# Kernel tuning notes

Measured on AMD Instinct MI355X. Metric: run time of the kernel, lower is better.

## Reference

```python
import jax, jax.numpy as jnp
import numpy as np

SEQ, BATCH, IN, HID, OUT = 512, 64, 512, 1024, 512
KEEP = 0.7  # dropout p = 0.3


def setup_inputs() -> dict:
    key = jax.random.key(0)
    ks = jax.random.split(key, 9)
    def lin(k, fan_out, fan_in):
        bound = 1.0 / np.sqrt(fan_in)
        kw, kb = jax.random.split(k)
        W = jax.random.uniform(kw, (fan_out, fan_in), jnp.float32, -bound, bound)
        b = jax.random.uniform(kb, (fan_out,), jnp.float32, -bound, bound)
        return W, b
    x = jax.random.normal(ks[0], (SEQ, BATCH, IN), jnp.float32)
    # inverted dropout mask, fixed for determinism
    drop_mask = (jax.random.bernoulli(ks[1], KEEP, (SEQ, BATCH, OUT))
                 .astype(jnp.float32) / KEEP)
    W_i2h, b_i2h = lin(ks[2], HID, IN + HID)
    W_i2o, b_i2o = lin(ks[3], OUT, IN + HID)
    W_o2o, b_o2o = lin(ks[4], OUT, HID + OUT)
    return {"x": x, "drop_mask": drop_mask,
            "W_i2h": W_i2h, "b_i2h": b_i2h,
            "W_i2o": W_i2o, "b_i2o": b_i2o,
            "W_o2o": W_o2o, "b_o2o": b_o2o}


def reference(x, drop_mask, W_i2h, b_i2h, W_i2o, b_i2o, W_o2o, b_o2o):
    # x: [S, B, IN]; returns log-probs [S, B, OUT]
    def step(h, inp):
        x_t, m_t = inp  # [B, IN], [B, OUT]
        comb = jnp.concatenate([x_t, h], axis=1)          # [B, IN+HID]
        out = comb @ W_i2o.T + b_i2o                      # [B, OUT]
        h_new = comb @ W_i2h.T + b_i2h                    # [B, HID]
        oc = jnp.concatenate([out, h_new], axis=1) @ W_o2o.T + b_o2o  # [B, OUT]
        oc = oc * m_t                                     # dropout (inverted mask)
        oc = jax.nn.log_softmax(oc, axis=-1)
        return h_new, oc
    h0 = jnp.zeros((x.shape[1], W_i2h.shape[0]), x.dtype)
    _, outs = jax.lax.scan(step, h0, (x, drop_mask))
    return outs
```

## Files before the change

### kernel.cpp

```cpp
#include <hip/hip_runtime.h>
#include <stdint.h>


typedef unsigned short ushort_t;
typedef __attribute__((ext_vector_type(8))) __bf16 bf16x8;
typedef __attribute__((ext_vector_type(4))) float f32x4;

__device__ __forceinline__ ushort_t f2bf(float f) {
  union { float f; uint32_t u; } v; v.f = f;
  uint32_t r = v.u + 0x7fffu + ((v.u >> 16) & 1u);
  return (ushort_t)(r >> 16);
}
__device__ __forceinline__ float bf2f(ushort_t b) {
  union { uint32_t u; float f; } v; v.u = ((uint32_t)b) << 16;
  return v.f;
}
__device__ __forceinline__ void gload16(const ushort_t* g, ushort_t* l) {
  __builtin_amdgcn_global_load_lds(
      (const __attribute__((address_space(1))) uint32_t*)g,
      (__attribute__((address_space(3))) uint32_t*)l, 16, 0, 0);
}

__global__ __launch_bounds__(256) void init_kernel(uint32_t* harr0) {
  int i = blockIdx.x * blockDim.x + threadIdx.x;
  if (i < 32768) harr0[i] = 0;
}

__global__ __launch_bounds__(256) void pack_kernel(
    const float* __restrict__ x, const float* __restrict__ mask,
    const float* __restrict__ W_i2h,
    const float* __restrict__ W_i2o, const float* __restrict__ W_o2o,
    const float* __restrict__ b_i2o, const float* __restrict__ b_o2o,
    ushort_t* xB, ushort_t* Wihx, ushort_t* Whh, ushort_t* Wiox,
    ushort_t* Wioh, ushort_t* Wo1, ushort_t* Wo2, float* biasP,
    uint64_t* maskb) {
  int64_t i = (int64_t)blockIdx.x * blockDim.x + threadIdx.x;
  const int64_t c0 = 16777216, c1 = 17301504, c2 = 18350080, c3 = 18612224,
                c4 = 19136512, c5 = 19398656, c6 = 19922944, c7 = 19923456,
                c8 = 36700672;
  if (i < c0) { xB[i] = f2bf(x[i]); return; }
  if (i < c1) { int64_t j = i - c0; int r = j >> 9,  c = j & 511;  Wihx[j] = f2bf(W_i2h[(int64_t)r * 1536 + c]); return; }
  if (i < c2) { int64_t j = i - c1; int r = j >> 10, c = j & 1023; Whh[j]  = f2bf(W_i2h[(int64_t)r * 1536 + 512 + c]); return; }
  if (i < c3) { int64_t j = i - c2; int r = j >> 9,  c = j & 511;  Wiox[j] = f2bf(W_i2o[(int64_t)r * 1536 + c]); return; }
  if (i < c4) { int64_t j = i - c3; int r = j >> 10, c = j & 1023; Wioh[j] = f2bf(W_i2o[(int64_t)r * 1536 + 512 + c]); return; }
  if (i < c5) { int64_t j = i - c4; int r = j >> 9,  c = j & 511;  Wo1[j]  = f2bf(W_o2o[(int64_t)r * 1536 + c]); return; }
  if (i < c6) { int64_t j = i - c5; int r = j >> 10, c = j & 1023; Wo2[j]  = f2bf(W_o2o[(int64_t)r * 1536 + 512 + c]); return; }
  if (i < c7) {
    int n = (int)(i - c6);
    const float* wr = W_o2o + (int64_t)n * 1536;
    float s = 0.f;
    for (int m = 0; m < 512; ++m) s += wr[m] * b_i2o[m];
    biasP[n] = s + b_o2o[n];
    return;
  }
  if (i < c8) {
    int64_t j = i - c7;
    float v = mask[j];
    uint64_t bits = __ballot(v != 0.0f);
    if ((j & 63) == 0) maskb[j >> 6] = bits;
  }
}

__global__ __launch_bounds__(256) void gemm_bt(
    const ushort_t* __restrict__ A1, int lda1, const ushort_t* __restrict__ B1, int K1,
    const float* __restrict__ bias, ushort_t* Cb, int Ntiles) {
  __shared__ __align__(16) ushort_t AsF[2][4096];
  __shared__ __align__(16) ushort_t BsF[2][4096];
  const int mt = blockIdx.x & 255, nt = blockIdx.x >> 8;
  const int m0 = mt * 128, n0 = nt * 128;
  const int tid = threadIdx.x;
  const int w = tid >> 6, l = tid & 63;
  const int quad = l >> 4, l15 = l & 15;
  const int wm = (w & 1) * 64, wn = (w >> 1) * 64;
  const int r0 = tid >> 2, chunk = tid & 3;
  f32x4 acc[4][4] = {};
  gload16(A1 + (size_t)(m0 + r0) * lda1 + chunk * 8,      &AsF[0][tid * 8]);
  gload16(A1 + (size_t)(m0 + r0 + 64) * lda1 + chunk * 8, &AsF[0][2048 + tid * 8]);
  gload16(B1 + (size_t)(n0 + r0) * K1 + chunk * 8,        &BsF[0][tid * 8]);
  gload16(B1 + (size_t)(n0 + r0 + 64) * K1 + chunk * 8,   &BsF[0][2048 + tid * 8]);
  const int NIT = K1 >> 5;
  for (int it = 0; it < NIT; ++it) {
    const int p = it & 1;
    __syncthreads();
    if (it + 1 < NIT) {
      const int kn = (it + 1) * 32;
      gload16(A1 + (size_t)(m0 + r0) * lda1 + kn + chunk * 8,      &AsF[p ^ 1][tid * 8]);
      gload16(A1 + (size_t)(m0 + r0 + 64) * lda1 + kn + chunk * 8, &AsF[p ^ 1][2048 + tid * 8]);
      gload16(B1 + (size_t)(n0 + r0) * K1 + kn + chunk * 8,        &BsF[p ^ 1][tid * 8]);
      gload16(B1 + (size_t)(n0 + r0 + 64) * K1 + kn + chunk * 8,   &BsF[p ^ 1][2048 + tid * 8]);
    }
    bf16x8 af[4], bfr[4];
#pragma unroll
    for (int i = 0; i < 4; ++i) af[i]  = *(const bf16x8*)&AsF[p][(wm + 16 * i + l15) * 32 + 8 * quad];
#pragma unroll
    for (int j = 0; j < 4; ++j) bfr[j] = *(const bf16x8*)&BsF[p][(wn + 16 * j + l15) * 32 + 8 * quad];
#pragma unroll
    for (int i = 0; i < 4; ++i)
#pragma unroll
      for (int j = 0; j < 4; ++j)
        acc[i][j] = __builtin_amdgcn_mfma_f32_16x16x32_bf16(af[i], bfr[j], acc[i][j], 0, 0, 0);
  }
  const int N = Ntiles * 128;
#pragma unroll
  for (int i = 0; i < 4; ++i) {
    const int row = m0 + wm + 16 * i + 4 * quad;
#pragma unroll
    for (int j = 0; j < 4; ++j) {
      const int col = n0 + wn + 16 * j + l15;
      const float bv = bias[col];
#pragma unroll
      for (int r = 0; r < 4; ++r)
        Cb[(size_t)(row + r) * N + col] = f2bf(acc[i][j][r] + bv);
    }
  }
}

__global__ __launch_bounds__(256) void usetup_kernel(
    const ushort_t* __restrict__ Wo1, const ushort_t* __restrict__ Wiox,
    const ushort_t* __restrict__ Wioh, ushort_t* __restrict__ U1,
    ushort_t* __restrict__ U2) {
  __shared__ __align__(16) ushort_t AsF[4096];
  __shared__ __align__(16) ushort_t BsF[4096];
  int job = blockIdx.x;
  const ushort_t* Bm; ushort_t* Om; int mt, nt, ldb;
  if (job < 16) { mt = job >> 2; nt = job & 3; Bm = Wiox; Om = U1; ldb = 512; }
  else { job -= 16; mt = job >> 3; nt = job & 7; Bm = Wioh; Om = U2; ldb = 1024; }
  const int m0 = mt * 128, n0 = nt * 128;
  const int tid = threadIdx.x;
  const int w = tid >> 6, l = tid & 63;
  const int quad = l >> 4, l15 = l & 15;
  const int wm = (w & 1) * 64, wn = (w >> 1) * 64;
  const int r0 = tid >> 2, chunk = tid & 3;
  f32x4 acc[4][4] = {};
  for (int k0 = 0; k0 < 512; k0 += 32) {
    __syncthreads();
    gload16(Wo1 + (size_t)(m0 + r0) * 512 + k0 + chunk * 8,      &AsF[tid * 8]);
    gload16(Wo1 + (size_t)(m0 + r0 + 64) * 512 + k0 + chunk * 8, &AsF[2048 + tid * 8]);
#pragma unroll
    for (int rep = 0; rep < 2; ++rep) {
      const int idx = tid + 256 * rep;
      const int kk = idx & 31, n8 = idx >> 5;
      union { uint4 v; ushort_t s[8]; } u;
      u.v = *(const uint4*)(Bm + (size_t)(k0 + kk) * ldb + n0 + n8 * 8);
#pragma unroll
      for (int i = 0; i < 8; ++i) BsF[(n8 * 8 + i) * 32 + kk] = u.s[i];
    }
    __syncthreads();
    bf16x8 af[4], bfr[4];
#pragma unroll
    for (int i = 0; i < 4; ++i) af[i]  = *(const bf16x8*)&AsF[(wm + 16 * i + l15) * 32 + 8 * quad];
#pragma unroll
    for (int j = 0; j < 4; ++j) bfr[j] = *(const bf16x8*)&BsF[(wn + 16 * j + l15) * 32 + 8 * quad];
#pragma unroll
    for (int i = 0; i < 4; ++i)
#pragma unroll
      for (int j = 0; j < 4; ++j)
        acc[i][j] = __builtin_amdgcn_mfma_f32_16x16x32_bf16(af[i], bfr[j], acc[i][j], 0, 0, 0);
  }
#pragma unroll
  for (int i = 0; i < 4; ++i) {
    const int row = m0 + wm + 16 * i + 4 * quad;
#pragma unroll
    for (int j = 0; j < 4; ++j) {
      const int col = n0 + wn + 16 * j + l15;
#pragma unroll
      for (int r = 0; r < 4; ++r)
        Om[(size_t)(row + r) * ldb + col] = f2bf(acc[i][j][r]);
    }
  }
}

__device__ void step_tile64(
    const ushort_t* __restrict__ A, const ushort_t* __restrict__ B, int n0,
    const ushort_t* __restrict__ X, ushort_t* __restrict__ O, int gate) {
  __shared__ __align__(16) ushort_t As[2][2048];
  __shared__ __align__(16) ushort_t Bs[2][4096];
  const int tid = threadIdx.x;
  const int w = tid >> 6, l = tid & 63;
  const int quad = l >> 4, l15 = l & 15;
  const int r0 = tid >> 2, chunk = tid & 3;
  f32x4 acc[4][2] = {};
  gload16(A + (size_t)r0 * 1024 + chunk * 8,             &As[0][tid * 8]);
  gload16(B + (size_t)(n0 + r0) * 1024 + chunk * 8,      &Bs[0][tid * 8]);
  gload16(B + (size_t)(n0 + r0 + 64) * 1024 + chunk * 8, &Bs[0][2048 + tid * 8]);
  for (int k0 = 0; k0 < 32; ++k0) {
    const int p = k0 & 1;
    __syncthreads();
    if (k0 < 31) {
      const int kn = (k0 + 1) * 32;
      gload16(A + (size_t)r0 * 1024 + kn + chunk * 8,             &As[p ^ 1][tid * 8]);
      gload16(B + (size_t)(n0 + r0) * 1024 + kn + chunk * 8,      &Bs[p ^ 1][tid * 8]);
      gload16(B + (size_t)(n0 + r0 + 64) * 1024 + kn + chunk * 8, &Bs[p ^ 1][2048 + tid * 8]);
    }
    bf16x8 af[4], bfr[2];
#pragma unroll
    for (int i = 0; i < 4; ++i) af[i]  = *(const bf16x8*)&As[p][(16 * i + l15) * 32 + 8 * quad];
#pragma unroll
    for (int j = 0; j < 2; ++j) bfr[j] = *(const bf16x8*)&Bs[p][(32 * w + 16 * j + l15) * 32 + 8 * quad];
#pragma unroll
    for (int i = 0; i < 4; ++i)
#pragma unroll
      for (int j = 0; j < 2; ++j)
        acc[i][j] = __builtin_amdgcn_mfma_f32_16x16x32_bf16(af[i], bfr[j], acc[i][j], 0, 0, 0);
  }
#pragma unroll
  for (int i = 0; i < 4; ++i) {
#pragma unroll
    for (int j = 0; j < 2; ++j) {
      const int col = n0 + 32 * w + 16 * j + l15;
#pragma unroll
      for (int r = 0; r < 4; ++r) {
        const int row = 16 * i + 4 * quad + r;
        const size_t idx = (size_t)row * 1024 + col;
        float v = gate ? acc[i][j][r] : 0.0f;
        O[idx] = f2bf(v + bf2f(X[idx]));
      }
    }
  }
}

__device__ void power_tile(const ushort_t* __restrict__ Am,
                           const ushort_t* __restrict__ Bm,
                           ushort_t* __restrict__ Om, int t) {
  __shared__ __align__(16) ushort_t AsF[4096];
  __shared__ __align__(16) ushort_t BsF[4096];
  const int mt = t >> 3, nt = t & 7;
  const int m0 = mt * 128, n0 = nt * 128;
  const int tid = threadIdx.x;
  const int w = tid >> 6, l = tid & 63;
  const int quad = l >> 4, l15 = l & 15;
  const int wm = (w & 1) * 64, wn = (w >> 1) * 64;
  const int r0 = tid >> 2, chunk = tid & 3;
  f32x4 acc[4][4] = {};
  for (int k0 = 0; k0 < 1024; k0 += 32) {
    __syncthreads();
    gload16(Am + (size_t)(m0 + r0) * 1024 + k0 + chunk * 8,      &AsF[tid * 8]);
    gload16(Am + (size_t)(m0 + r0 + 64) * 1024 + k0 + chunk * 8, &AsF[2048 + tid * 8]);
#pragma unroll
    for (int rep = 0; rep < 2; ++rep) {
      const int idx = tid + 256 * rep;
      const int kk = idx & 31, n8 = idx >> 5;
      union { uint4 v; ushort_t s[8]; } u;
      u.v = *(const uint4*)(Bm + (size_t)(k0 + kk) * 1024 + n0 + n8 * 8);
#pragma unroll
      for (int i = 0; i < 8; ++i) BsF[(n8 * 8 + i) * 32 + kk] = u.s[i];
    }
    __syncthreads();
    bf16x8 af[4], bfr[4];
#pragma unroll
    for (int i = 0; i < 4; ++i) af[i]  = *(const bf16x8*)&AsF[(wm + 16 * i + l15) * 32 + 8 * quad];
#pragma unroll
    for (int j = 0; j < 4; ++j) bfr[j] = *(const bf16x8*)&BsF[(wn + 16 * j + l15) * 32 + 8 * quad];
#pragma unroll
    for (int i = 0; i < 4; ++i)
#pragma unroll
      for (int j = 0; j < 4; ++j)
        acc[i][j] = __builtin_amdgcn_mfma_f32_16x16x32_bf16(af[i], bfr[j], acc[i][j], 0, 0, 0);
  }
#pragma unroll
  for (int i = 0; i < 4; ++i) {
    const int row = m0 + wm + 16 * i + 4 * quad;
#pragma unroll
    for (int j = 0; j < 4; ++j) {
      const int col = n0 + wn + 16 * j + l15;
#pragma unroll
      for (int r = 0; r < 4; ++r)
        Om[(size_t)(row + r) * 1024 + col] = f2bf(acc[i][j][r]);
    }
  }
}

#define PWp(idx) (Pw + (size_t)(idx) * 1048576)

__global__ __launch_bounds__(256) void step_pow(
    const ushort_t* __restrict__ A, const ushort_t* __restrict__ X,
    ushort_t* __restrict__ O, const ushort_t* __restrict__ Whh,
    ushort_t* __restrict__ Pw, int mode) {
  const int bid = blockIdx.x;
  if (mode == 8 || bid >= 512) {
    const int q = (mode == 8) ? bid : bid - 512;
    const int pj = q >> 6, t = q & 63;
    const ushort_t *Am, *Bm; ushort_t* Om;
    switch (mode) {
      case 1:  Am = Whh;     Bm = Whh;     Om = PWp(0);  break;
      case 2:  if (pj == 0) { Am = Whh;    Bm = PWp(0);  Om = PWp(1); }
               else         { Am = PWp(0); Bm = PWp(0);  Om = PWp(2); }
               break;
      case 3:  if (pj == 0)      { Am = Whh;    Bm = PWp(2); Om = PWp(3); }
               else if (pj == 1) { Am = PWp(0); Bm = PWp(2); Om = PWp(4); }
               else if (pj == 2) { Am = PWp(1); Bm = PWp(2); Om = PWp(5); }
               else              { Am = PWp(2); Bm = PWp(2); Om = PWp(6); }
               break;
      case 4:  Am = PWp(6);  Bm = PWp(6);  Om = PWp(7);  break;
      case 5:  Am = PWp(7);  Bm = PWp(7);  Om = PWp(8);  break;
      case 6:  Am = PWp(8);  Bm = PWp(8);  Om = PWp(9);  break;
      case 7:  Am = PWp(9);  Bm = PWp(9);  Om = PWp(10); break;
      default: Am = PWp(10); Bm = PWp(10); Om = PWp(11); break;
    }
    power_tile(Am, Bm, Om, t);
    return;
  }
  const int c = bid >> 3, nt = bid & 7;
  step_tile64(A + (size_t)c * 524288, Whh, nt * 128,
              X + (size_t)c * 524288, O + (size_t)c * 524288, 1);
}

__global__ __launch_bounds__(256) void scan64(
    const ushort_t* __restrict__ old, ushort_t* __restrict__ nw,
    const ushort_t* __restrict__ Pv, int d) {
  const int c = blockIdx.x >> 3, nt = blockIdx.x & 7;
  const int ia = (c >= d) ? (c - d) : c;
  step_tile64(old + (size_t)ia * 524288, Pv, nt * 128,
              old + (size_t)c * 524288, nw + (size_t)c * 524288, c >= d);
}

__global__ __launch_bounds__(256) void correct_kernel(
    const ushort_t* __restrict__ S, const ushort_t* __restrict__ XhB,
    ushort_t* __restrict__ Harr, const ushort_t* __restrict__ Whh,
    const ushort_t* __restrict__ Pw) {
  __shared__ __align__(16) ushort_t AsF[2][4096];
  __shared__ __align__(16) ushort_t BsF[2][4096];
  const int p_ = blockIdx.x >> 3;
  const int n0 = (blockIdx.x & 7) * 128;
  const int j = blockIdx.y + 1;
  const ushort_t* Wj = (j == 1) ? Whh : (Pw + (size_t)(j - 2) * 1048576);
  const ushort_t* Xs = (j == 1) ? XhB : (Harr + (size_t)j * 65536);
  ushort_t* XO = Harr + (size_t)j * 65536;
  const int tid = threadIdx.x;
  const int w = tid >> 6, l = tid & 63;
  const int quad = l >> 4, l15 = l & 15;
  const int wm = (w & 1) * 64, wn = (w >> 1) * 64;
  const int r0 = tid >> 2, chunk = tid & 3;
  f32x4 acc[4][4] = {};
  const ushort_t* a0 = S + (size_t)(2 * p_) * 524288 + (size_t)r0 * 1024;
  const ushort_t* a1 = S + (size_t)(2 * p_ + 1) * 524288 + (size_t)r0 * 1024;
  gload16(a0 + chunk * 8, &AsF[0][tid * 8]);
  gload16(a1 + chunk * 8, &AsF[0][2048 + tid * 8]);
  gload16(Wj + (size_t)(n0 + r0) * 1024 + chunk * 8,      &BsF[0][tid * 8]);
  gload16(Wj + (size_t)(n0 + r0 + 64) * 1024 + chunk * 8, &BsF[0][2048 + tid * 8]);
  for (int it = 0; it < 32; ++it) {
    const int p = it & 1;
    __syncthreads();
    if (it < 31) {
      const int kn = (it + 1) * 32;
      gload16(a0 + kn + chunk * 8, &AsF[p ^ 1][tid * 8]);
      gload16(a1 + kn + chunk * 8, &AsF[p ^ 1][2048 + tid * 8]);
      gload16(Wj + (size_t)(n0 + r0) * 1024 + kn + chunk * 8,      &BsF[p ^ 1][tid * 8]);
      gload16(Wj + (size_t)(n0 + r0 + 64) * 1024 + kn + chunk * 8, &BsF[p ^ 1][2048 + tid * 8]);
    }
    bf16x8 af[4], bfr[4];
#pragma unroll
    for (int i = 0; i < 4; ++i) af[i]  = *(const bf16x8*)&AsF[p][(wm + 16 * i + l15) * 32 + 8 * quad];
#pragma unroll
    for (int jj = 0; jj < 4; ++jj) bfr[jj] = *(const bf16x8*)&BsF[p][(wn + 16 * jj + l15) * 32 + 8 * quad];
#pragma unroll
    for (int i = 0; i < 4; ++i)
#pragma unroll
      for (int jj = 0; jj < 4; ++jj)
        acc[i][jj] = __builtin_amdgcn_mfma_f32_16x16x32_bf16(af[i], bfr[jj], acc[i][jj], 0, 0, 0);
  }
#pragma unroll
  for (int i = 0; i < 4; ++i) {
#pragma unroll
    for (int jj = 0; jj < 4; ++jj) {
      const int col = n0 + wn + 16 * jj + l15;
#pragma unroll
      for (int r = 0; r < 4; ++r) {
        const int gr = wm + 16 * i + 4 * quad + r;
        const int c = 2 * p_ + (gr >> 6);
        const size_t idx = (size_t)c * 524288 + (size_t)(gr & 63) * 1024 + col;
        XO[idx] = f2bf(acc[i][jj][r] + bf2f(Xs[idx]));
      }
    }
  }
}

__global__ __launch_bounds__(256) void gemm_fused(
    const ushort_t* __restrict__ xB, const ushort_t* __restrict__ U1,
    const ushort_t* __restrict__ Harr, const ushort_t* __restrict__ U2,
    const ushort_t* __restrict__ Wo2, const float* __restrict__ biasP,
    const uint64_t* __restrict__ maskb, float* __restrict__ out) {
  __shared__ __align__(16) ushort_t AsF[2][4096];
  __shared__ __align__(16) ushort_t BsF[2][4096];
  const int mt = blockIdx.x & 255, nt = blockIdx.x >> 8;
  const int m0 = mt * 128, n0 = nt * 128;
  const int tid = threadIdx.x;
  const int w = tid >> 6, l = tid & 63;
  const int quad = l >> 4, l15 = l & 15;
  const int wm = (w & 1) * 64, wn = (w >> 1) * 64;
  const int r0 = tid >> 2, chunk = tid & 3;
  f32x4 acc[4][4] = {};
  auto issue = [&](int it, int b) {
    const ushort_t *A, *B; int K, k0;
    if (it < 16)      { A = xB;           B = U1;  K = 512;  k0 = it << 5; }
    else if (it < 48) { A = Harr;         B = U2;  K = 1024; k0 = (it - 16) << 5; }
    else              { A = Harr + 65536; B = Wo2; K = 1024; k0 = (it - 48) << 5; }
    gload16(A + (size_t)(m0 + r0) * K + k0 + chunk * 8,      &AsF[b][tid * 8]);
    gload16(A + (size_t)(m0 + r0 + 64) * K + k0 + chunk * 8, &AsF[b][2048 + tid * 8]);
    gload16(B + (size_t)(n0 + r0) * K + k0 + chunk * 8,      &BsF[b][tid * 8]);
    gload16(B + (size_t)(n0 + r0 + 64) * K + k0 + chunk * 8, &BsF[b][2048 + tid * 8]);
  };
  issue(0, 0);
  for (int it = 0; it < 80; ++it) {
    const int p = it & 1;
    __syncthreads();
    if (it < 79) issue(it + 1, p ^ 1);
    bf16x8 af[4], bfr[4];
#pragma unroll
    for (int i = 0; i < 4; ++i) af[i]  = *(const bf16x8*)&AsF[p][(wm + 16 * i + l15) * 32 + 8 * quad];
#pragma unroll
    for (int j = 0; j < 4; ++j) bfr[j] = *(const bf16x8*)&BsF[p][(wn + 16 * j + l15) * 32 + 8 * quad];
#pragma unroll
    for (int i = 0; i < 4; ++i)
#pragma unroll
      for (int j = 0; j < 4; ++j)
        acc[i][j] = __builtin_amdgcn_mfma_f32_16x16x32_bf16(af[i], bfr[j], acc[i][j], 0, 0, 0);
  }
  const float INV_KEEP = 1.0f / 0.7f;
#pragma unroll
  for (int i = 0; i < 4; ++i) {
    const int row = m0 + wm + 16 * i + 4 * quad;
#pragma unroll
    for (int j = 0; j < 4; ++j) {
      const int col = n0 + wn + 16 * j + l15;
      const float bv = biasP[col];
#pragma unroll
      for (int r = 0; r < 4; ++r) {
        const size_t idx = (size_t)(row + r) * 512 + col;
        const uint64_t bits = maskb[idx >> 6];
        out[idx] = ((bits >> (idx & 63)) & 1) ? (acc[i][j][r] + bv) * INV_KEEP
                                              : 0.0f;
      }
    }
  }
}

__global__ __launch_bounds__(256) void softmax_kernel(float* __restrict__ out) {
  const int row = blockIdx.x;
  const int tid = threadIdx.x;
  const size_t base = (size_t)row * 512;
  __shared__ float sm[4], ss[4];
  const float v0 = out[base + tid];
  const float v1 = out[base + tid + 256];
  float m = fmaxf(v0, v1);
#pragma unroll
  for (int off = 32; off; off >>= 1) m = fmaxf(m, __shfl_xor(m, off, 64));
  const int w = tid >> 6;
  if ((tid & 63) == 0) sm[w] = m;
  __syncthreads();
  m = fmaxf(fmaxf(sm[0], sm[1]), fmaxf(sm[2], sm[3]));
  float s = __expf(v0 - m) + __expf(v1 - m);
#pragma unroll
  for (int off = 32; off; off >>= 1) s += __shfl_xor(s, off, 64);
  if ((tid & 63) == 0) ss[w] = s;
  __syncthreads();
  s = ss[0] + ss[1] + ss[2] + ss[3];
  const float lg = logf(s);
  out[base + tid] = v0 - m - lg;
  out[base + tid + 256] = v1 - m - lg;
}

extern "C" void kernel_launch(void* const* d_in, const int* in_sizes, int n_in,
                              void* d_out, int out_size, void* d_ws, size_t ws_size,
                              hipStream_t stream) {
  const float* x     = (const float*)d_in[0];
  const float* mask  = (const float*)d_in[1];
  const float* W_i2h = (const float*)d_in[2];
  const float* b_i2h = (const float*)d_in[3];
  const float* W_i2o = (const float*)d_in[4];
  const float* b_i2o = (const float*)d_in[5];
  const float* W_o2o = (const float*)d_in[6];
  const float* b_o2o = (const float*)d_in[7];
  float* out = (float*)d_out;

  char* ws = (char*)d_ws;
  const size_t NEED = 207749120;
  if (ws_size < NEED) return;
  ushort_t* xB   = (ushort_t*)(ws + 0);
  ushort_t* XhB  = (ushort_t*)(ws + 33554432);
  ushort_t* SA   = XhB + 65536;
  ushort_t* SB   = XhB + 3 * 65536;
  ushort_t* Harr = (ushort_t*)(ws + 100663296);
  ushort_t* Pw   = (ushort_t*)(ws + 167903232);
  ushort_t* U1   = (ushort_t*)(ws + 193069056);
  ushort_t* U2   = (ushort_t*)(ws + 193593344);
  float* biasP   = (float*)(ws + 194641920);
  uint64_t* maskb = (uint64_t*)(ws + 195000320);
  ushort_t* Wihx = (ushort_t*)(ws + 201457664);
  ushort_t* Whh  = (ushort_t*)(ws + 202506240);
  ushort_t* Wiox = (ushort_t*)(ws + 204603392);
  ushort_t* Wioh = (ushort_t*)(ws + 205127680);
  ushort_t* Wo1  = (ushort_t*)(ws + 206176256);
  ushort_t* Wo2  = (ushort_t*)(ws + 206700544);

  hipLaunchKernelGGL(init_kernel, dim3(128), dim3(256), 0, stream, (uint32_t*)Harr);
  hipLaunchKernelGGL(pack_kernel, dim3(143362), dim3(256), 0, stream,
                     x, mask, W_i2h, W_i2o, W_o2o, b_i2o, b_o2o,
                     xB, Wihx, Whh, Wiox, Wioh, Wo1, Wo2, biasP, maskb);
  hipLaunchKernelGGL(gemm_bt, dim3(2048), dim3(256), 0, stream,
                     xB, 512, Wihx, 512, b_i2h, XhB, 8);
  hipLaunchKernelGGL(usetup_kernel, dim3(48), dim3(256), 0, stream,
                     Wo1, Wiox, Wioh, U1, U2);
  const int extraP[8] = {0, 64, 128, 256, 64, 64, 64, 64};
  for (int k = 1; k <= 7; ++k) {
    const ushort_t* A = (k == 1) ? XhB : (Harr + (size_t)k * 65536);
    hipLaunchKernelGGL(step_pow, dim3(512 + extraP[k]), dim3(256), 0, stream,
                       A, XhB + (size_t)k * 65536, Harr + (size_t)(k + 1) * 65536,
                       Whh, Pw, k);
  }
  hipLaunchKernelGGL(step_pow, dim3(64), dim3(256), 0, stream,
                     Whh, Whh, (ushort_t*)Harr, Whh, Pw, 8);
  hipLaunchKernelGGL(scan64, dim3(512), dim3(256), 0, stream, Harr, SB, Pw + 6 * 1048576, 1);
  hipLaunchKernelGGL(scan64, dim3(512), dim3(256), 0, stream, SB, SA, Pw + 7 * 1048576, 2);
  hipLaunchKernelGGL(scan64, dim3(512), dim3(256), 0, stream, SA, SB, Pw + 8 * 1048576, 4);
  hipLaunchKernelGGL(scan64, dim3(512), dim3(256), 0, stream, SB, SA, Pw + 9 * 1048576, 8);
  hipLaunchKernelGGL(scan64, dim3(512), dim3(256), 0, stream, SA, SB, Pw + 10 * 1048576, 16);
  hipLaunchKernelGGL(scan64, dim3(512), dim3(256), 0, stream, SB, SA, Pw + 11 * 1048576, 32);
  hipLaunchKernelGGL(correct_kernel, dim3(dim3(256, 8)), dim3(256), 0, stream,
                     SA, XhB, Harr, Whh, Pw);
  hipLaunchKernelGGL(gemm_fused, dim3(1024), dim3(256), 0, stream,
                     xB, U1, Harr, U2, Wo2, biasP, maskb, out);
  hipLaunchKernelGGL(softmax_kernel, dim3(32768), dim3(256), 0, stream, out);
}
```

Before: 1.035 ms.

## Restructure recurrence into fewer wider passes and fold power GEMMs into scans

Replaces the seven sequential step_pow launches plus a separate power launch with three pass kernels. Each pass computes several hidden-state chunks in parallel using precomputed powers of Whh, with a two-term accumulation where needed. Each later matrix power is folded into the preceding scan launch, the usetup GEMM is merged into gemm_bt, and scan blocks with c<d now do a plain copy instead of a gated zero GEMM. The aim is to shorten the serial kernel chain and cut wasted MFMA work, in exchange for more complex dependency ordering between launches and shared-memory reuse across heterogeneous blocks.

```diff
diff --git a/kernel.cpp b/kernel.cpp
--- a/kernel.cpp
+++ b/kernel.cpp
@@ -61,67 +61,12 @@
   }
 }
 
-__global__ __launch_bounds__(256) void gemm_bt(
-    const ushort_t* __restrict__ A1, int lda1, const ushort_t* __restrict__ B1, int K1,
-    const float* __restrict__ bias, ushort_t* Cb, int Ntiles) {
-  __shared__ __align__(16) ushort_t AsF[2][4096];
-  __shared__ __align__(16) ushort_t BsF[2][4096];
-  const int mt = blockIdx.x & 255, nt = blockIdx.x >> 8;
-  const int m0 = mt * 128, n0 = nt * 128;
-  const int tid = threadIdx.x;
-  const int w = tid >> 6, l = tid & 63;
-  const int quad = l >> 4, l15 = l & 15;
-  const int wm = (w & 1) * 64, wn = (w >> 1) * 64;
-  const int r0 = tid >> 2, chunk = tid & 3;
-  f32x4 acc[4][4] = {};
-  gload16(A1 + (size_t)(m0 + r0) * lda1 + chunk * 8,      &AsF[0][tid * 8]);
-  gload16(A1 + (size_t)(m0 + r0 + 64) * lda1 + chunk * 8, &AsF[0][2048 + tid * 8]);
-  gload16(B1 + (size_t)(n0 + r0) * K1 + chunk * 8,        &BsF[0][tid * 8]);
-  gload16(B1 + (size_t)(n0 + r0 + 64) * K1 + chunk * 8,   &BsF[0][2048 + tid * 8]);
-  const int NIT = K1 >> 5;
-  for (int it = 0; it < NIT; ++it) {
-    const int p = it & 1;
-    __syncthreads();
-    if (it + 1 < NIT) {
-      const int kn = (it + 1) * 32;
-      gload16(A1 + (size_t)(m0 + r0) * lda1 + kn + chunk * 8,      &AsF[p ^ 1][tid * 8]);
-      gload16(A1 + (size_t)(m0 + r0 + 64) * lda1 + kn + chunk * 8, &AsF[p ^ 1][2048 + tid * 8]);
-      gload16(B1 + (size_t)(n0 + r0) * K1 + kn + chunk * 8,        &BsF[p ^ 1][tid * 8]);
-      gload16(B1 + (size_t)(n0 + r0 + 64) * K1 + kn + chunk * 8,   &BsF[p ^ 1][2048 + tid * 8]);
-    }
-    bf16x8 af[4], bfr[4];
-#pragma unroll
-    for (int i = 0; i < 4; ++i) af[i]  = *(const bf16x8*)&AsF[p][(wm + 16 * i + l15) * 32 + 8 * quad];
-#pragma unroll
-    for (int j = 0; j < 4; ++j) bfr[j] = *(const bf16x8*)&BsF[p][(wn + 16 * j + l15) * 32 + 8 * quad];
-#pragma unroll
-    for (int i = 0; i < 4; ++i)
-#pragma unroll
-      for (int j = 0; j < 4; ++j)
-        acc[i][j] = __builtin_amdgcn_mfma_f32_16x16x32_bf16(af[i], bfr[j], acc[i][j], 0, 0, 0);
-  }
-  const int N = Ntiles * 128;
-#pragma unroll
-  for (int i = 0; i < 4; ++i) {
-    const int row = m0 + wm + 16 * i + 4 * quad;
-#pragma unroll
-    for (int j = 0; j < 4; ++j) {
-      const int col = n0 + wn + 16 * j + l15;
-      const float bv = bias[col];
-#pragma unroll
-      for (int r = 0; r < 4; ++r)
-        Cb[(size_t)(row + r) * N + col] = f2bf(acc[i][j][r] + bv);
-    }
-  }
-}
-
-__global__ __launch_bounds__(256) void usetup_kernel(
+__device__ void usetup_tile(ushort_t* SH,
     const ushort_t* __restrict__ Wo1, const ushort_t* __restrict__ Wiox,
     const ushort_t* __restrict__ Wioh, ushort_t* __restrict__ U1,
-    ushort_t* __restrict__ U2) {
-  __shared__ __align__(16) ushort_t AsF[4096];
-  __shared__ __align__(16) ushort_t BsF[4096];
-  int job = blockIdx.x;
+    ushort_t* __restrict__ U2, int job) {
+  ushort_t* AsF = SH;
+  ushort_t* BsF = SH + 4096;
   const ushort_t* Bm; ushort_t* Om; int mt, nt, ldb;
   if (job < 16) { mt = job >> 2; nt = job & 3; Bm = Wiox; Om = U1; ldb = 512; }
   else { job -= 16; mt = job >> 3; nt = job & 7; Bm = Wioh; Om = U2; ldb = 1024; }
@@ -170,33 +115,98 @@
   }
 }
 
-__device__ void step_tile64(
-    const ushort_t* __restrict__ A, const ushort_t* __restrict__ B, int n0,
-    const ushort_t* __restrict__ X, ushort_t* __restrict__ O, int gate) {
-  __shared__ __align__(16) ushort_t As[2][2048];
-  __shared__ __align__(16) ushort_t Bs[2][4096];
+__global__ __launch_bounds__(256) void gemm_bt(
+    const ushort_t* __restrict__ A1, int lda1, const ushort_t* __restrict__ B1, int K1,
+    const float* __restrict__ bias, ushort_t* Cb, int Ntiles,
+    const ushort_t* __restrict__ Wo1, const ushort_t* __restrict__ Wiox,
+    const ushort_t* __restrict__ Wioh, ushort_t* __restrict__ U1,
+    ushort_t* __restrict__ U2) {
+  __shared__ __align__(16) ushort_t SH[16384];
+  if (blockIdx.x >= 2048) {
+    usetup_tile(SH, Wo1, Wiox, Wioh, U1, U2, blockIdx.x - 2048);
+    return;
+  }
+  const int mt = blockIdx.x & 255, nt = blockIdx.x >> 8;
+  const int m0 = mt * 128, n0 = nt * 128;
+  const int tid = threadIdx.x;
+  const int w = tid >> 6, l = tid & 63;
+  const int quad = l >> 4, l15 = l & 15;
+  const int wm = (w & 1) * 64, wn = (w >> 1) * 64;
+  const int r0 = tid >> 2, chunk = tid & 3;
+  f32x4 acc[4][4] = {};
+  gload16(A1 + (size_t)(m0 + r0) * lda1 + chunk * 8,      &SH[tid * 8]);
+  gload16(A1 + (size_t)(m0 + r0 + 64) * lda1 + chunk * 8, &SH[2048 + tid * 8]);
+  gload16(B1 + (size_t)(n0 + r0) * K1 + chunk * 8,        &SH[8192 + tid * 8]);
+  gload16(B1 + (size_t)(n0 + r0 + 64) * K1 + chunk * 8,   &SH[8192 + 2048 + tid * 8]);
+  const int NIT = K1 >> 5;
+  for (int it = 0; it < NIT; ++it) {
+    const int p = it & 1;
+    const int ao = p * 4096, bo = 8192 + p * 4096;
+    __syncthreads();
+    if (it + 1 < NIT) {
+      const int kn = (it + 1) * 32;
+      const int an = (p ^ 1) * 4096, bn = 8192 + (p ^ 1) * 4096;
+      gload16(A1 + (size_t)(m0 + r0) * lda1 + kn + chunk * 8,      &SH[an + tid * 8]);
+      gload16(A1 + (size_t)(m0 + r0 + 64) * lda1 + kn + chunk * 8, &SH[an + 2048 + tid * 8]);
+      gload16(B1 + (size_t)(n0 + r0) * K1 + kn + chunk * 8,        &SH[bn + tid * 8]);
+      gload16(B1 + (size_t)(n0 + r0 + 64) * K1 + kn + chunk * 8,   &SH[bn + 2048 + tid * 8]);
+    }
+    bf16x8 af[4], bfr[4];
+#pragma unroll
+    for (int i = 0; i < 4; ++i) af[i]  = *(const bf16x8*)&SH[ao + (wm + 16 * i + l15) * 32 + 8 * quad];
+#pragma unroll
+    for (int j = 0; j < 4; ++j) bfr[j] = *(const bf16x8*)&SH[bo + (wn + 16 * j + l15) * 32 + 8 * quad];
+#pragma unroll
+    for (int i = 0; i < 4; ++i)
+#pragma unroll
+      for (int j = 0; j < 4; ++j)
+        acc[i][j] = __builtin_amdgcn_mfma_f32_16x16x32_bf16(af[i], bfr[j], acc[i][j], 0, 0, 0);
+  }
+  const int N = Ntiles * 128;
+#pragma unroll
+  for (int i = 0; i < 4; ++i) {
+    const int row = m0 + wm + 16 * i + 4 * quad;
+#pragma unroll
+    for (int j = 0; j < 4; ++j) {
+      const int col = n0 + wn + 16 * j + l15;
+      const float bv = bias[col];
+#pragma unroll
+      for (int r = 0; r < 4; ++r)
+        Cb[(size_t)(row + r) * N + col] = f2bf(acc[i][j][r] + bv);
+    }
+  }
+}
+
+__device__ void step_tile64m(ushort_t* SH,
+    const ushort_t* __restrict__ A0, const ushort_t* __restrict__ B0,
+    const ushort_t* __restrict__ A1, const ushort_t* __restrict__ B1,
+    int nterms, int n0, const ushort_t* X, ushort_t* O) {
   const int tid = threadIdx.x;
   const int w = tid >> 6, l = tid & 63;
   const int quad = l >> 4, l15 = l & 15;
   const int r0 = tid >> 2, chunk = tid & 3;
   f32x4 acc[4][2] = {};
-  gload16(A + (size_t)r0 * 1024 + chunk * 8,             &As[0][tid * 8]);
-  gload16(B + (size_t)(n0 + r0) * 1024 + chunk * 8,      &Bs[0][tid * 8]);
-  gload16(B + (size_t)(n0 + r0 + 64) * 1024 + chunk * 8, &Bs[0][2048 + tid * 8]);
-  for (int k0 = 0; k0 < 32; ++k0) {
-    const int p = k0 & 1;
-    __syncthreads();
-    if (k0 < 31) {
-      const int kn = (k0 + 1) * 32;
-      gload16(A + (size_t)r0 * 1024 + kn + chunk * 8,             &As[p ^ 1][tid * 8]);
-      gload16(B + (size_t)(n0 + r0) * 1024 + kn + chunk * 8,      &Bs[p ^ 1][tid * 8]);
-      gload16(B + (size_t)(n0 + r0 + 64) * 1024 + kn + chunk * 8, &Bs[p ^ 1][2048 + tid * 8]);
-    }
+  const int NIT = nterms << 5;
+  auto issue = [&](int it, int b) {
+    const ushort_t* A = (it >= 32) ? A1 : A0;
+    const ushort_t* B = (it >= 32) ? B1 : B0;
+    const int kk = (it & 31) * 32;
+    const int ab = b * 2048, bb = 4096 + b * 4096;
+    gload16(A + (size_t)r0 * 1024 + kk + chunk * 8,             &SH[ab + tid * 8]);
+    gload16(B + (size_t)(n0 + r0) * 1024 + kk + chunk * 8,      &SH[bb + tid * 8]);
+    gload16(B + (size_t)(n0 + r0 + 64) * 1024 + kk + chunk * 8, &SH[bb + 2048 + tid * 8]);
+  };
+  issue(0, 0);
+  for (int it = 0; it < NIT; ++it) {
+    const int p = it & 1;
+    const int ap = p * 2048, bp = 4096 + p * 4096;
+    __syncthreads();
+    if (it + 1 < NIT) issue(it + 1, p ^ 1);
     bf16x8 af[4], bfr[2];
 #pragma unroll
-    for (int i = 0; i < 4; ++i) af[i]  = *(const bf16x8*)&As[p][(16 * i + l15) * 32 + 8 * quad];
-#pragma unroll
-    for (int j = 0; j < 2; ++j) bfr[j] = *(const bf16x8*)&Bs[p][(32 * w + 16 * j + l15) * 32 + 8 * quad];
+    for (int i = 0; i < 4; ++i) af[i]  = *(const bf16x8*)&SH[ap + (16 * i + l15) * 32 + 8 * quad];
+#pragma unroll
+    for (int j = 0; j < 2; ++j) bfr[j] = *(const bf16x8*)&SH[bp + (32 * w + 16 * j + l15) * 32 + 8 * quad];
 #pragma unroll
     for (int i = 0; i < 4; ++i)
 #pragma unroll
@@ -212,18 +222,25 @@
       for (int r = 0; r < 4; ++r) {
         const int row = 16 * i + 4 * quad + r;
         const size_t idx = (size_t)row * 1024 + col;
-        float v = gate ? acc[i][j][r] : 0.0f;
-        O[idx] = f2bf(v + bf2f(X[idx]));
+        O[idx] = f2bf(acc[i][j][r] + bf2f(X[idx]));
       }
     }
   }
 }
 
-__device__ void power_tile(const ushort_t* __restrict__ Am,
+__device__ void copy_tile(const ushort_t* X, ushort_t* O, int n0) {
+  const int t = threadIdx.x, r = t >> 2, q = t & 3;
+  const uint4* src = (const uint4*)(X + (size_t)r * 1024 + n0 + q * 32);
+  uint4* dst = (uint4*)(O + (size_t)r * 1024 + n0 + q * 32);
+  dst[0] = src[0]; dst[1] = src[1]; dst[2] = src[2]; dst[3] = src[3];
+}
+
+__device__ void power_tile(ushort_t* SH,
+                           const ushort_t* __restrict__ Am,
                            const ushort_t* __restrict__ Bm,
                            ushort_t* __restrict__ Om, int t) {
-  __shared__ __align__(16) ushort_t AsF[4096];
-  __shared__ __align__(16) ushort_t BsF[4096];
+  ushort_t* AsF = SH;
+  ushort_t* BsF = SH + 4096;
   const int mt = t >> 3, nt = t & 7;
   const int m0 = mt * 128, n0 = nt * 128;
   const int tid = threadIdx.x;
@@ -272,46 +289,72 @@
 
 #define PWp(idx) (Pw + (size_t)(idx) * 1048576)
 
-__global__ __launch_bounds__(256) void step_pow(
-    const ushort_t* __restrict__ A, const ushort_t* __restrict__ X,
-    ushort_t* __restrict__ O, const ushort_t* __restrict__ Whh,
-    ushort_t* __restrict__ Pw, int mode) {
+__global__ __launch_bounds__(256) void pass_kernel(
+    const ushort_t* __restrict__ XhB, ushort_t* __restrict__ Harr,
+    const ushort_t* __restrict__ Whh, ushort_t* __restrict__ Pw, int mode) {
+  __shared__ __align__(16) ushort_t SH[12288];
   const int bid = blockIdx.x;
-  if (mode == 8 || bid >= 512) {
-    const int q = (mode == 8) ? bid : bid - 512;
+  const int nunits = (mode == 2) ? 3 : 4;
+  if (bid >= nunits * 512) {
+    const int q = bid - nunits * 512;
     const int pj = q >> 6, t = q & 63;
     const ushort_t *Am, *Bm; ushort_t* Om;
-    switch (mode) {
-      case 1:  Am = Whh;     Bm = Whh;     Om = PWp(0);  break;
-      case 2:  if (pj == 0) { Am = Whh;    Bm = PWp(0);  Om = PWp(1); }
-               else         { Am = PWp(0); Bm = PWp(0);  Om = PWp(2); }
-               break;
-      case 3:  if (pj == 0)      { Am = Whh;    Bm = PWp(2); Om = PWp(3); }
-               else if (pj == 1) { Am = PWp(0); Bm = PWp(2); Om = PWp(4); }
-               else if (pj == 2) { Am = PWp(1); Bm = PWp(2); Om = PWp(5); }
-               else              { Am = PWp(2); Bm = PWp(2); Om = PWp(6); }
-               break;
-      case 4:  Am = PWp(6);  Bm = PWp(6);  Om = PWp(7);  break;
-      case 5:  Am = PWp(7);  Bm = PWp(7);  Om = PWp(8);  break;
-      case 6:  Am = PWp(8);  Bm = PWp(8);  Om = PWp(9);  break;
-      case 7:  Am = PWp(9);  Bm = PWp(9);  Om = PWp(10); break;
-      default: Am = PWp(10); Bm = PWp(10); Om = PWp(11); break;
-    }
-    power_tile(Am, Bm, Om, t);
+    if (mode == 1)      { Am = Whh;    Bm = Whh;    Om = PWp(0); }
+    else if (mode == 2) {
+      if (pj == 0) { Am = Whh;    Bm = PWp(0); Om = PWp(1); }
+      else         { Am = PWp(0); Bm = PWp(0); Om = PWp(2); }
+    } else {
+      switch (pj) {
+        case 0:  Am = Whh;    Bm = PWp(2); Om = PWp(3); break;
+        case 1:  Am = PWp(0); Bm = PWp(2); Om = PWp(4); break;
+        case 2:  Am = PWp(1); Bm = PWp(2); Om = PWp(5); break;
+        default: Am = PWp(2); Bm = PWp(2); Om = PWp(6); break;
+      }
+    }
+    power_tile(SH, Am, Bm, Om, t);
     return;
   }
-  const int c = bid >> 3, nt = bid & 7;
-  step_tile64(A + (size_t)c * 524288, Whh, nt * 128,
-              X + (size_t)c * 524288, O + (size_t)c * 524288, 1);
+  const int u = bid >> 9, inner = bid & 511;
+  const int c = inner >> 3, n0 = (inner & 7) * 128;
+  const size_t co = (size_t)c * 524288;
+#define HS_(s) (Harr + (size_t)(s) * 65536)
+#define XS_(s) (XhB + (size_t)(s) * 65536)
+  const ushort_t *A0, *B0, *A1 = nullptr, *B1 = nullptr, *X; ushort_t* O;
+  int terms = 1;
+  if (mode == 1) {
+    const int as[4] = {0, 2, 4, 6}, xs[4] = {1, 3, 5, 7}, os[4] = {2, 4, 1, 8};
+    A0 = XS_(as[u]); B0 = Whh; X = XS_(xs[u]); O = HS_(os[u]);
+  } else if (mode == 2) {
+    if (u == 0)      { A0 = HS_(2); B0 = Whh;    X = XS_(2); O = HS_(3); }
+    else if (u == 1) { A0 = HS_(2); B0 = PWp(0); X = HS_(4); O = HS_(4); }
+    else             { A0 = HS_(1); B0 = PWp(0); X = HS_(8); O = HS_(8); }
+  } else {
+    if (u == 0)      { A0 = HS_(4); B0 = Whh;    X = XS_(4); O = HS_(5); }
+    else if (u == 1) { A0 = HS_(4); B0 = PWp(0); X = HS_(1); O = HS_(6); }
+    else if (u == 2) { A0 = HS_(1); B0 = Whh; A1 = HS_(4); B1 = PWp(1);
+                       terms = 2;               X = XS_(6); O = HS_(7); }
+    else             { A0 = HS_(4); B0 = PWp(2); X = HS_(8); O = HS_(8); }
+  }
+  step_tile64m(SH, A0 + co, B0, A1 ? A1 + co : nullptr, B1, terms, n0,
+               X + co, O + co);
 }
 
 __global__ __launch_bounds__(256) void scan64(
     const ushort_t* __restrict__ old, ushort_t* __restrict__ nw,
-    const ushort_t* __restrict__ Pv, int d) {
-  const int c = blockIdx.x >> 3, nt = blockIdx.x & 7;
-  const int ia = (c >= d) ? (c - d) : c;
-  step_tile64(old + (size_t)ia * 524288, Pv, nt * 128,
-              old + (size_t)c * 524288, nw + (size_t)c * 524288, c >= d);
+    const ushort_t* __restrict__ Pv, int d,
+    const ushort_t* __restrict__ Pra, ushort_t* __restrict__ Pwo) {
+  __shared__ __align__(16) ushort_t SH[12288];
+  if (blockIdx.x >= 512) {
+    power_tile(SH, Pra, Pra, Pwo, blockIdx.x - 512);
+    return;
+  }
+  const int c = blockIdx.x >> 3, n0 = (blockIdx.x & 7) * 128;
+  if (c < d) {
+    copy_tile(old + (size_t)c * 524288, nw + (size_t)c * 524288, n0);
+    return;
+  }
+  step_tile64m(SH, old + (size_t)(c - d) * 524288, Pv, nullptr, nullptr, 1, n0,
+               old + (size_t)c * 524288, nw + (size_t)c * 524288);
 }
 
 __global__ __launch_bounds__(256) void correct_kernel(
@@ -497,25 +540,21 @@
   hipLaunchKernelGGL(pack_kernel, dim3(143362), dim3(256), 0, stream,
                      x, mask, W_i2h, W_i2o, W_o2o, b_i2o, b_o2o,
                      xB, Wihx, Whh, Wiox, Wioh, Wo1, Wo2, biasP, maskb);
-  hipLaunchKernelGGL(gemm_bt, dim3(2048), dim3(256), 0, stream,
-                     xB, 512, Wihx, 512, b_i2h, XhB, 8);
-  hipLaunchKernelGGL(usetup_kernel, dim3(48), dim3(256), 0, stream,
+  hipLaunchKernelGGL(gemm_bt, dim3(2096), dim3(256), 0, stream,
+                     xB, 512, Wihx, 512, b_i2h, XhB, 8,
                      Wo1, Wiox, Wioh, U1, U2);
-  const int extraP[8] = {0, 64, 128, 256, 64, 64, 64, 64};
-  for (int k = 1; k <= 7; ++k) {
-    const ushort_t* A = (k == 1) ? XhB : (Harr + (size_t)k * 65536);
-    hipLaunchKernelGGL(step_pow, dim3(512 + extraP[k]), dim3(256), 0, stream,
-                       A, XhB + (size_t)k * 65536, Harr + (size_t)(k + 1) * 65536,
-                       Whh, Pw, k);
-  }
-  hipLaunchKernelGGL(step_pow, dim3(64), dim3(256), 0, stream,
-                     Whh, Whh, (ushort_t*)Harr, Whh, Pw, 8);
-  hipLaunchKernelGGL(scan64, dim3(512), dim3(256), 0, stream, Harr, SB, Pw + 6 * 1048576, 1);
-  hipLaunchKernelGGL(scan64, dim3(512), dim3(256), 0, stream, SB, SA, Pw + 7 * 1048576, 2);
-  hipLaunchKernelGGL(scan64, dim3(512), dim3(256), 0, stream, SA, SB, Pw + 8 * 1048576, 4);
-  hipLaunchKernelGGL(scan64, dim3(512), dim3(256), 0, stream, SB, SA, Pw + 9 * 1048576, 8);
-  hipLaunchKernelGGL(scan64, dim3(512), dim3(256), 0, stream, SA, SB, Pw + 10 * 1048576, 16);
-  hipLaunchKernelGGL(scan64, dim3(512), dim3(256), 0, stream, SB, SA, Pw + 11 * 1048576, 32);
+  hipLaunchKernelGGL(pass_kernel, dim3(2112), dim3(256), 0, stream,
+                     XhB, Harr, Whh, Pw, 1);
+  hipLaunchKernelGGL(pass_kernel, dim3(1664), dim3(256), 0, stream,
+                     XhB, Harr, Whh, Pw, 2);
+  hipLaunchKernelGGL(pass_kernel, dim3(2304), dim3(256), 0, stream,
+                     XhB, Harr, Whh, Pw, 3);
+  hipLaunchKernelGGL(scan64, dim3(576), dim3(256), 0, stream, Harr, SB, PWp(6),  1, PWp(6),  PWp(7));
+  hipLaunchKernelGGL(scan64, dim3(576), dim3(256), 0, stream, SB, SA, PWp(7),  2, PWp(7),  PWp(8));
+  hipLaunchKernelGGL(scan64, dim3(576), dim3(256), 0, stream, SA, SB, PWp(8),  4, PWp(8),  PWp(9));
+  hipLaunchKernelGGL(scan64, dim3(576), dim3(256), 0, stream, SB, SA, PWp(9),  8, PWp(9),  PWp(10));
+  hipLaunchKernelGGL(scan64, dim3(576), dim3(256), 0, stream, SA, SB, PWp(10), 16, PWp(10), PWp(11));
+  hipLaunchKernelGGL(scan64, dim3(512), dim3(256), 0, stream, SB, SA, PWp(11), 32, (const ushort_t*)nullptr, (ushort_t*)nullptr);
   hipLaunchKernelGGL(correct_kernel, dim3(dim3(256, 8)), dim3(256), 0, stream,
                      SA, XhB, Harr, Whh, Pw);
   hipLaunchKernelGGL(gemm_fused, dim3(1024), dim3(256), 0, stream,
```

Result: slower. 1.472 ms (+42.1%).
